# Kernel optimization log

Hardware: AMD Instinct MI355X
Metric: run time of the kernel (lower is better)

The kernel has to match this reference:

```python
import jax, jax.numpy as jnp
import numpy as np

D_IN = 1024
D_OUT = 1024
B = 4
S = 2048


def setup_inputs() -> dict:
    key = jax.random.key(0)
    kx, kq, kk, kv = jax.random.split(key, 4)
    x = jax.random.normal(kx, (B, S, D_IN), dtype=jnp.float32)
    # Linear weights stored as [d_in, d_out] so projection is x @ W
    sc = 1.0 / np.sqrt(D_IN)
    Wq = jax.random.normal(kq, (D_IN, D_OUT), dtype=jnp.float32) * sc
    Wk = jax.random.normal(kk, (D_IN, D_OUT), dtype=jnp.float32) * sc
    Wv = jax.random.normal(kv, (D_IN, D_OUT), dtype=jnp.float32) * sc
    return {"x": x, "Wq": Wq, "Wk": Wk, "Wv": Wv}


def reference(x, Wq, Wk, Wv):
    # q, k, v: [b, s, d_out]
    q = jnp.einsum("bsd,de->bse", x, Wq)
    k = jnp.einsum("bsd,de->bse", x, Wk)
    v = jnp.einsum("bsd,de->bse", x, Wv)
    s = q.shape[1]
    # raw scores [b, s, s]
    scores = jnp.einsum("bqd,bkd->bqk", q, k)
    # causal mask: disallow key j > query i (see notes re: original mask bug)
    causal = jnp.triu(jnp.ones((s, s), dtype=bool), k=1)
    scores = jnp.where(causal[None, :, :], -jnp.inf, scores)
    scale = 1.0 / jnp.sqrt(jnp.asarray(k.shape[-1], dtype=scores.dtype))
    att_weights = jax.nn.softmax(scores * scale, axis=-1)
    # dropout p=0.0 -> identity
    att_output = jnp.einsum("bqk,bkd->bqd", att_weights, v)
    return att_output, att_weights
```

## Files before the change

kernel.cpp:

```cpp
#include <hip/hip_runtime.h>
#include <stdint.h>

#define DIM 1024
#define SEQ 2048
#define NB 4

typedef unsigned short u16;
typedef __bf16 bf16x8 __attribute__((ext_vector_type(8)));
typedef float floatx4 __attribute__((ext_vector_type(4)));

__device__ __forceinline__ u16 f32_to_bf16(float f) {
  union { float f; unsigned u; } v; v.f = f;
  unsigned r = v.u + 0x7FFFu + ((v.u >> 16) & 1u);
  return (u16)(r >> 16);
}

__device__ __forceinline__ void async16(const void* g, void* l) {
  __builtin_amdgcn_global_load_lds(
      (__attribute__((address_space(1))) unsigned int*)g,
      (__attribute__((address_space(3))) unsigned int*)l, 16, 0, 0);
}

__global__ __launch_bounds__(256) void k_cvt(const float* __restrict__ src,
                                             u16* __restrict__ dst, int n4) {
  int i = blockIdx.x * blockDim.x + threadIdx.x;
  if (i >= n4) return;
  float4 v = ((const float4*)src)[i];
  ushort4 o;
  o.x = f32_to_bf16(v.x); o.y = f32_to_bf16(v.y);
  o.z = f32_to_bf16(v.z); o.w = f32_to_bf16(v.w);
  ((ushort4*)dst)[i] = o;
}

__global__ void k_tr_f32(const float* __restrict__ Wq, const float* __restrict__ Wk,
                         const float* __restrict__ Wv, u16* __restrict__ dst) {
  const int z = blockIdx.z;
  const float* src = (z == 0) ? Wq : (z == 1) ? Wk : Wv;
  u16* d = dst + (size_t)z * DIM * DIM;
  __shared__ u16 tile[32][33];
  int c0 = blockIdx.x * 32, r0 = blockIdx.y * 32;
  int tx = threadIdx.x, ty = threadIdx.y;
  #pragma unroll
  for (int dy = 0; dy < 32; dy += 8)
    tile[ty + dy][tx] = f32_to_bf16(src[(size_t)(r0 + ty + dy) * DIM + c0 + tx]);
  __syncthreads();
  #pragma unroll
  for (int dy = 0; dy < 32; dy += 8)
    d[(size_t)(c0 + ty + dy) * DIM + r0 + tx] = tile[tx][ty + dy];
}

__device__ __forceinline__ void mfma_core(const u16* __restrict__ A, int lda,
                                          const u16* __restrict__ Bt, int ldb,
                                          int ktiles, u16* lds,
                                          floatx4 acc[4][4]) {
  const int tid = threadIdx.x;
  const int lane = tid & 63;
  const int wid = tid >> 6;
  u16* lds_a = lds;
  u16* lds_b = lds + 8192;

  const u16* ag = A + (size_t)(wid * 32 + (lane >> 3)) * lda + (lane & 7) * 8;
  const u16* bg = Bt + (size_t)(wid * 32 + (lane >> 3)) * ldb + (lane & 7) * 8;
  u16* la = lds_a + wid * 2048;
  u16* lb = lds_b + wid * 2048;

  const int wm = (wid >> 1) * 64, wn = (wid & 1) * 64;
  const int lrow = lane & 15, quad = lane >> 4;
  const u16* pa = lds_a + (wm + lrow) * 64 + quad * 8;
  const u16* pb = lds_b + (wn + lrow) * 64 + quad * 8;

  for (int kt = 0; kt < ktiles; ++kt) {
    #pragma unroll
    for (int c = 0; c < 4; ++c) {
      async16(ag + (size_t)c * 8 * lda, la + c * 512);
      async16(bg + (size_t)c * 8 * ldb, lb + c * 512);
    }
    ag += 64; bg += 64;
    __syncthreads();
    #pragma unroll
    for (int ks = 0; ks < 2; ++ks) {
      bf16x8 af[4], bfr[4];
      #pragma unroll
      for (int t = 0; t < 4; ++t) af[t] = *(const bf16x8*)(pa + t * 1024 + ks * 32);
      #pragma unroll
      for (int t = 0; t < 4; ++t) bfr[t] = *(const bf16x8*)(pb + t * 1024 + ks * 32);
      #pragma unroll
      for (int i = 0; i < 4; ++i)
        #pragma unroll
        for (int j = 0; j < 4; ++j)
          acc[i][j] = __builtin_amdgcn_mfma_f32_16x16x32_bf16(af[i], bfr[j],
                                                              acc[i][j], 0, 0, 0);
    }
    __syncthreads();
  }
}

__global__ __launch_bounds__(256) void k_projqk(const u16* __restrict__ xb,
                                                const u16* __restrict__ wt,
                                                u16* __restrict__ qk) {
  const int x = blockIdx.x;
  const int mt = (x >> 7) * 8 + (x & 7);
  const int nt = (x >> 3) & 15;
  __shared__ u16 lds[16384];
  floatx4 acc[4][4] = {};
  mfma_core(xb + (size_t)mt * 128 * DIM, DIM,
            wt + (size_t)nt * 128 * DIM, DIM, DIM / 64, lds, acc);
  const int lane = threadIdx.x & 63, wid = threadIdx.x >> 6;
  const int wm = (wid >> 1) * 64, wn = (wid & 1) * 64;
  const int lrow = lane & 15, quad = lane >> 4;
  const int n0 = nt * 128;
  const int z = n0 >> 10;
  const int nn = n0 & 1023;
  u16* C = qk + (size_t)z * (NB * SEQ * DIM)
              + (size_t)(mt * 128 + wm + quad * 4) * DIM + nn + wn + lrow;
  #pragma unroll
  for (int i = 0; i < 4; ++i)
    #pragma unroll
    for (int r = 0; r < 4; ++r)
      #pragma unroll
      for (int j = 0; j < 4; ++j)
        C[(size_t)(i * 16 + r) * DIM + j * 16] = f32_to_bf16(acc[i][j][r]);
}

__global__ __launch_bounds__(256) void k_projv(const u16* __restrict__ wv,
                                               const u16* __restrict__ xb,
                                               u16* __restrict__ vT) {
  const int x = blockIdx.x;
  const int nt = (x >> 6) * 8 + (x & 7);
  const int mt = (x >> 3) & 7;
  __shared__ u16 lds[16384];
  floatx4 acc[4][4] = {};
  mfma_core(wv + (size_t)mt * 128 * DIM, DIM,
            xb + (size_t)nt * 128 * DIM, DIM, DIM / 64, lds, acc);
  const int lane = threadIdx.x & 63, wid = threadIdx.x >> 6;
  const int wm = (wid >> 1) * 64, wn = (wid & 1) * 64;
  const int lrow = lane & 15, quad = lane >> 4;
  const int t0 = nt * 128;
  const int b = t0 >> 11, s0 = t0 & 2047;
  u16* C = vT + (size_t)b * (DIM * SEQ)
              + (size_t)(mt * 128 + wm + quad * 4) * SEQ + s0 + wn + lrow;
  #pragma unroll
  for (int i = 0; i < 4; ++i)
    #pragma unroll
    for (int r = 0; r < 4; ++r)
      #pragma unroll
      for (int j = 0; j < 4; ++j)
        C[(size_t)(i * 16 + r) * SEQ + j * 16] = f32_to_bf16(acc[i][j][r]);
}

__global__ __launch_bounds__(256) void k_scores(const u16* __restrict__ q,
                                                const u16* __restrict__ k,
                                                float* __restrict__ w) {
  const int id = blockIdx.x;
  const int b = (id & 7) >> 1;
  const int mtl = id & 1;
  const int rest = id >> 3;
  const int mt = (rest >> 4) * 2 + mtl;
  const int nt = rest & 15;
  if (nt > mt) return;
  __shared__ u16 lds[16384];
  floatx4 acc[4][4] = {};
  mfma_core(q + (size_t)b * SEQ * DIM + (size_t)mt * 128 * DIM, DIM,
            k + (size_t)b * SEQ * DIM + (size_t)nt * 128 * DIM, DIM,
            DIM / 64, lds, acc);
  const int lane = threadIdx.x & 63, wid = threadIdx.x >> 6;
  const int wm = (wid >> 1) * 64, wn = (wid & 1) * 64;
  const int lrow = lane & 15, quad = lane >> 4;
  float* C = w + (size_t)b * SEQ * SEQ
               + (size_t)(mt * 128 + wm + quad * 4) * SEQ + nt * 128 + wn + lrow;
  #pragma unroll
  for (int i = 0; i < 4; ++i)
    #pragma unroll
    for (int r = 0; r < 4; ++r)
      #pragma unroll
      for (int j = 0; j < 4; ++j)
        C[(size_t)(i * 16 + r) * SEQ + j * 16] = acc[i][j][r] * 0.03125f;
}

__global__ __launch_bounds__(256) void k_softmax(float* __restrict__ w,
                                                 u16* __restrict__ P) {
  const int r = blockIdx.x;
  const int i = r & (SEQ - 1);
  const int len = i + 1;
  const int plen4 = (((i >> 7) + 1) << 7) >> 2;
  float4* srow = (float4*)(w + (size_t)r * SEQ);
  ushort4* prow = (ushort4*)(P + (size_t)r * SEQ);
  const int tid = threadIdx.x;
  const int lane = tid & 63, wid = tid >> 6;
  __shared__ float rm[4], rs[4];

  float4 e[2];
  float mx = -1e30f;
  #pragma unroll
  for (int u = 0; u < 2; ++u) {
    int q4 = tid + u * 256;
    int j0 = q4 * 4;
    float4 v = make_float4(-1e30f, -1e30f, -1e30f, -1e30f);
    if (j0 < len) {
      v = srow[q4];
      v.x = (j0 + 0 < len) ? v.x : -1e30f;
      v.y = (j0 + 1 < len) ? v.y : -1e30f;
      v.z = (j0 + 2 < len) ? v.z : -1e30f;
      v.w = (j0 + 3 < len) ? v.w : -1e30f;
    }
    e[u] = v;
    mx = fmaxf(mx, fmaxf(fmaxf(v.x, v.y), fmaxf(v.z, v.w)));
  }
  #pragma unroll
  for (int o = 32; o >= 1; o >>= 1) mx = fmaxf(mx, __shfl_xor(mx, o, 64));
  if (lane == 0) rm[wid] = mx;
  __syncthreads();
  mx = fmaxf(fmaxf(rm[0], rm[1]), fmaxf(rm[2], rm[3]));

  float sum = 0.f;
  #pragma unroll
  for (int u = 0; u < 2; ++u) {
    e[u].x = __expf(e[u].x - mx);
    e[u].y = __expf(e[u].y - mx);
    e[u].z = __expf(e[u].z - mx);
    e[u].w = __expf(e[u].w - mx);
    sum += e[u].x + e[u].y + e[u].z + e[u].w;
  }
  #pragma unroll
  for (int o = 32; o >= 1; o >>= 1) sum += __shfl_xor(sum, o, 64);
  if (lane == 0) rs[wid] = sum;
  __syncthreads();
  sum = rs[0] + rs[1] + rs[2] + rs[3];
  const float inv = 1.0f / sum;

  #pragma unroll
  for (int u = 0; u < 2; ++u) {
    int q4 = tid + u * 256;
    int j0 = q4 * 4;
    float4 v;
    v.x = (j0 + 0 < len) ? e[u].x * inv : 0.f;
    v.y = (j0 + 1 < len) ? e[u].y * inv : 0.f;
    v.z = (j0 + 2 < len) ? e[u].z * inv : 0.f;
    v.w = (j0 + 3 < len) ? e[u].w * inv : 0.f;
    srow[q4] = v;
    if (q4 < plen4) {
      ushort4 p;
      p.x = f32_to_bf16(v.x); p.y = f32_to_bf16(v.y);
      p.z = f32_to_bf16(v.z); p.w = f32_to_bf16(v.w);
      prow[q4] = p;
    }
  }
}

__global__ __launch_bounds__(256) void k_pv(const u16* __restrict__ P,
                                            const u16* __restrict__ vT,
                                            float* __restrict__ out) {
  const int id = blockIdx.x;
  const int b = (id & 7) >> 1;
  const int mtl = id & 1;
  const int rest = id >> 3;
  const int mt = (rest >> 3) * 2 + mtl;
  const int nt = rest & 7;
  __shared__ u16 lds[16384];
  floatx4 acc[4][4] = {};
  mfma_core(P + (size_t)b * SEQ * SEQ + (size_t)mt * 128 * SEQ, SEQ,
            vT + (size_t)b * DIM * SEQ + (size_t)nt * 128 * SEQ, SEQ,
            2 * (mt + 1), lds, acc);
  const int lane = threadIdx.x & 63, wid = threadIdx.x >> 6;
  const int wm = (wid >> 1) * 64, wn = (wid & 1) * 64;
  const int lrow = lane & 15, quad = lane >> 4;
  float* C = out + (size_t)b * SEQ * DIM
                 + (size_t)(mt * 128 + wm + quad * 4) * DIM + nt * 128 + wn + lrow;
  #pragma unroll
  for (int i = 0; i < 4; ++i)
    #pragma unroll
    for (int r = 0; r < 4; ++r)
      #pragma unroll
      for (int j = 0; j < 4; ++j)
        C[(size_t)(i * 16 + r) * DIM + j * 16] = acc[i][j][r];
}

extern "C" void kernel_launch(void* const* d_in, const int* in_sizes, int n_in,
                              void* d_out, int out_size, void* d_ws, size_t ws_size,
                              hipStream_t stream) {
  const float* x  = (const float*)d_in[0];
  const float* Wq = (const float*)d_in[1];
  const float* Wk = (const float*)d_in[2];
  const float* Wv = (const float*)d_in[3];
  float* att_out = (float*)d_out;
  float* att_w   = (float*)d_out + 8388608;

  u16* xb = (u16*)d_ws;
  u16* wt = xb + 8388608;
  u16* qk = wt + 3145728;
  u16* vT = qk + 16777216;
  u16* P  = vT + 8388608;

  dim3 tb(32, 8);
  k_cvt<<<8192, 256, 0, stream>>>(x, xb, 8388608 / 4);
  k_tr_f32<<<dim3(32, 32, 3), tb, 0, stream>>>(Wq, Wk, Wv, wt);
  k_projqk<<<1024, 256, 0, stream>>>(xb, wt, qk);
  k_projv<<<512, 256, 0, stream>>>(wt + 2097152, xb, vT);
  k_scores<<<1024, 256, 0, stream>>>(qk, qk + 8388608, att_w);
  k_softmax<<<8192, 256, 0, stream>>>(att_w, P);
  k_pv<<<512, 256, 0, stream>>>(P, vT, att_out);
}
```

Baseline: 316.7 us.

## Merge prep and projection launches, compact causal score grid, reorder PV blocks

Combines the x conversion and weight transpose into one launch, and the Q/K and V projections into one 1536-block launch, removing launch gaps and tail effects between them. The scores grid shrinks from 1024 blocks (half exiting early) to 544 blocks covering only lower-triangular tiles, using a sqrt-based triangular index. The PV kernel now schedules the longest row tiles first to improve load balance. Risks include losing the previous L2-friendly block swizzle and some integer/sqrt overhead per block.

```diff
diff --git a/kernel.cpp b/kernel.cpp
--- a/kernel.cpp
+++ b/kernel.cpp
@@ -21,32 +21,38 @@
       (__attribute__((address_space(3))) unsigned int*)l, 16, 0, 0);
 }
 
-__global__ __launch_bounds__(256) void k_cvt(const float* __restrict__ src,
-                                             u16* __restrict__ dst, int n4) {
-  int i = blockIdx.x * blockDim.x + threadIdx.x;
-  if (i >= n4) return;
-  float4 v = ((const float4*)src)[i];
-  ushort4 o;
-  o.x = f32_to_bf16(v.x); o.y = f32_to_bf16(v.y);
-  o.z = f32_to_bf16(v.z); o.w = f32_to_bf16(v.w);
-  ((ushort4*)dst)[i] = o;
-}
-
-__global__ void k_tr_f32(const float* __restrict__ Wq, const float* __restrict__ Wk,
-                         const float* __restrict__ Wv, u16* __restrict__ dst) {
-  const int z = blockIdx.z;
-  const float* src = (z == 0) ? Wq : (z == 1) ? Wk : Wv;
-  u16* d = dst + (size_t)z * DIM * DIM;
+__global__ __launch_bounds__(256) void k_prep(const float* __restrict__ x,
+                                              const float* __restrict__ Wq,
+                                              const float* __restrict__ Wk,
+                                              const float* __restrict__ Wv,
+                                              u16* __restrict__ xb,
+                                              u16* __restrict__ wt) {
   __shared__ u16 tile[32][33];
-  int c0 = blockIdx.x * 32, r0 = blockIdx.y * 32;
-  int tx = threadIdx.x, ty = threadIdx.y;
-  #pragma unroll
-  for (int dy = 0; dy < 32; dy += 8)
-    tile[ty + dy][tx] = f32_to_bf16(src[(size_t)(r0 + ty + dy) * DIM + c0 + tx]);
-  __syncthreads();
-  #pragma unroll
-  for (int dy = 0; dy < 32; dy += 8)
-    d[(size_t)(c0 + ty + dy) * DIM + r0 + tx] = tile[tx][ty + dy];
+  const int bid = blockIdx.x;
+  const int tid = threadIdx.x;
+  if (bid < 8192) {
+    int i = bid * 256 + tid;
+    float4 v = ((const float4*)x)[i];
+    ushort4 o;
+    o.x = f32_to_bf16(v.x); o.y = f32_to_bf16(v.y);
+    o.z = f32_to_bf16(v.z); o.w = f32_to_bf16(v.w);
+    ((ushort4*)xb)[i] = o;
+  } else {
+    int t = bid - 8192;
+    int z = t >> 10;
+    int ti = t & 1023;
+    int c0 = (ti & 31) * 32, r0 = (ti >> 5) * 32;
+    const float* src = (z == 0) ? Wq : (z == 1) ? Wk : Wv;
+    u16* d = wt + (size_t)z * DIM * DIM;
+    int tx = tid & 31, ty = tid >> 5;
+    #pragma unroll
+    for (int dy = 0; dy < 32; dy += 8)
+      tile[ty + dy][tx] = f32_to_bf16(src[(size_t)(r0 + ty + dy) * DIM + c0 + tx]);
+    __syncthreads();
+    #pragma unroll
+    for (int dy = 0; dy < 32; dy += 8)
+      d[(size_t)(c0 + ty + dy) * DIM + r0 + tx] = tile[tx][ty + dy];
+  }
 }
 
 __device__ __forceinline__ void mfma_core(const u16* __restrict__ A, int lda,
@@ -95,69 +101,64 @@
   }
 }
 
-__global__ __launch_bounds__(256) void k_projqk(const u16* __restrict__ xb,
-                                                const u16* __restrict__ wt,
-                                                u16* __restrict__ qk) {
-  const int x = blockIdx.x;
-  const int mt = (x >> 7) * 8 + (x & 7);
-  const int nt = (x >> 3) & 15;
+__global__ __launch_bounds__(256) void k_proj(const u16* __restrict__ xb,
+                                              const u16* __restrict__ wt,
+                                              u16* __restrict__ qk,
+                                              u16* __restrict__ vT) {
+  const int id = blockIdx.x;
+  const int z2 = id >> 9;
+  const int r = id & 511;
+  const int g = (r >> 6) * 8 + (r & 7);
+  const int h = (r >> 3) & 7;
   __shared__ u16 lds[16384];
   floatx4 acc[4][4] = {};
-  mfma_core(xb + (size_t)mt * 128 * DIM, DIM,
-            wt + (size_t)nt * 128 * DIM, DIM, DIM / 64, lds, acc);
+  const u16 *A, *Bt;
+  if (z2 < 2) {
+    A = xb + (size_t)g * 128 * DIM;
+    Bt = wt + (size_t)z2 * DIM * DIM + (size_t)h * 128 * DIM;
+  } else {
+    A = wt + (size_t)2 * DIM * DIM + (size_t)h * 128 * DIM;
+    Bt = xb + (size_t)g * 128 * DIM;
+  }
+  mfma_core(A, DIM, Bt, DIM, DIM / 64, lds, acc);
   const int lane = threadIdx.x & 63, wid = threadIdx.x >> 6;
   const int wm = (wid >> 1) * 64, wn = (wid & 1) * 64;
   const int lrow = lane & 15, quad = lane >> 4;
-  const int n0 = nt * 128;
-  const int z = n0 >> 10;
-  const int nn = n0 & 1023;
-  u16* C = qk + (size_t)z * (NB * SEQ * DIM)
-              + (size_t)(mt * 128 + wm + quad * 4) * DIM + nn + wn + lrow;
-  #pragma unroll
-  for (int i = 0; i < 4; ++i)
-    #pragma unroll
-    for (int r = 0; r < 4; ++r)
-      #pragma unroll
-      for (int j = 0; j < 4; ++j)
-        C[(size_t)(i * 16 + r) * DIM + j * 16] = f32_to_bf16(acc[i][j][r]);
-}
-
-__global__ __launch_bounds__(256) void k_projv(const u16* __restrict__ wv,
-                                               const u16* __restrict__ xb,
-                                               u16* __restrict__ vT) {
-  const int x = blockIdx.x;
-  const int nt = (x >> 6) * 8 + (x & 7);
-  const int mt = (x >> 3) & 7;
-  __shared__ u16 lds[16384];
-  floatx4 acc[4][4] = {};
-  mfma_core(wv + (size_t)mt * 128 * DIM, DIM,
-            xb + (size_t)nt * 128 * DIM, DIM, DIM / 64, lds, acc);
-  const int lane = threadIdx.x & 63, wid = threadIdx.x >> 6;
-  const int wm = (wid >> 1) * 64, wn = (wid & 1) * 64;
-  const int lrow = lane & 15, quad = lane >> 4;
-  const int t0 = nt * 128;
-  const int b = t0 >> 11, s0 = t0 & 2047;
-  u16* C = vT + (size_t)b * (DIM * SEQ)
-              + (size_t)(mt * 128 + wm + quad * 4) * SEQ + s0 + wn + lrow;
-  #pragma unroll
-  for (int i = 0; i < 4; ++i)
-    #pragma unroll
-    for (int r = 0; r < 4; ++r)
-      #pragma unroll
-      for (int j = 0; j < 4; ++j)
-        C[(size_t)(i * 16 + r) * SEQ + j * 16] = f32_to_bf16(acc[i][j][r]);
+  if (z2 < 2) {
+    u16* C = qk + (size_t)z2 * (NB * SEQ * DIM)
+                + (size_t)(g * 128 + wm + quad * 4) * DIM + h * 128 + wn + lrow;
+    #pragma unroll
+    for (int i = 0; i < 4; ++i)
+      #pragma unroll
+      for (int rr = 0; rr < 4; ++rr)
+        #pragma unroll
+        for (int j = 0; j < 4; ++j)
+          C[(size_t)(i * 16 + rr) * DIM + j * 16] = f32_to_bf16(acc[i][j][rr]);
+  } else {
+    const int t0 = g * 128;
+    const int b = t0 >> 11, s0 = t0 & 2047;
+    u16* C = vT + (size_t)b * (DIM * SEQ)
+                + (size_t)(h * 128 + wm + quad * 4) * SEQ + s0 + wn + lrow;
+    #pragma unroll
+    for (int i = 0; i < 4; ++i)
+      #pragma unroll
+      for (int rr = 0; rr < 4; ++rr)
+        #pragma unroll
+        for (int j = 0; j < 4; ++j)
+          C[(size_t)(i * 16 + rr) * SEQ + j * 16] = f32_to_bf16(acc[i][j][rr]);
+  }
 }
 
 __global__ __launch_bounds__(256) void k_scores(const u16* __restrict__ q,
                                                 const u16* __restrict__ k,
                                                 float* __restrict__ w) {
   const int id = blockIdx.x;
-  const int b = (id & 7) >> 1;
-  const int mtl = id & 1;
-  const int rest = id >> 3;
-  const int mt = (rest >> 4) * 2 + mtl;
-  const int nt = rest & 15;
-  if (nt > mt) return;
+  const int b = id & 3;
+  int t = id >> 2;
+  int mt = (int)((sqrtf(8.0f * (float)t + 1.0f) - 1.0f) * 0.5f);
+  while ((mt + 1) * (mt + 2) / 2 <= t) ++mt;
+  while (mt * (mt + 1) / 2 > t) --mt;
+  const int nt = t - mt * (mt + 1) / 2;
   __shared__ u16 lds[16384];
   floatx4 acc[4][4] = {};
   mfma_core(q + (size_t)b * SEQ * DIM + (size_t)mt * 128 * DIM, DIM,
@@ -171,10 +172,10 @@
   #pragma unroll
   for (int i = 0; i < 4; ++i)
     #pragma unroll
-    for (int r = 0; r < 4; ++r)
+    for (int rr = 0; rr < 4; ++rr)
       #pragma unroll
       for (int j = 0; j < 4; ++j)
-        C[(size_t)(i * 16 + r) * SEQ + j * 16] = acc[i][j][r] * 0.03125f;
+        C[(size_t)(i * 16 + rr) * SEQ + j * 16] = acc[i][j][rr] * 0.03125f;
 }
 
 __global__ __launch_bounds__(256) void k_softmax(float* __restrict__ w,
@@ -251,11 +252,9 @@
                                             const u16* __restrict__ vT,
                                             float* __restrict__ out) {
   const int id = blockIdx.x;
-  const int b = (id & 7) >> 1;
-  const int mtl = id & 1;
-  const int rest = id >> 3;
-  const int mt = (rest >> 3) * 2 + mtl;
-  const int nt = rest & 7;
+  const int mt = 15 - (id >> 5);
+  const int nt = (id >> 2) & 7;
+  const int b = id & 3;
   __shared__ u16 lds[16384];
   floatx4 acc[4][4] = {};
   mfma_core(P + (size_t)b * SEQ * SEQ + (size_t)mt * 128 * SEQ, SEQ,
@@ -269,10 +268,10 @@
   #pragma unroll
   for (int i = 0; i < 4; ++i)
     #pragma unroll
-    for (int r = 0; r < 4; ++r)
+    for (int rr = 0; rr < 4; ++rr)
       #pragma unroll
       for (int j = 0; j < 4; ++j)
-        C[(size_t)(i * 16 + r) * DIM + j * 16] = acc[i][j][r];
+        C[(size_t)(i * 16 + rr) * DIM + j * 16] = acc[i][j][rr];
 }
 
 extern "C" void kernel_launch(void* const* d_in, const int* in_sizes, int n_in,
@@ -291,12 +290,9 @@
   u16* vT = qk + 16777216;
   u16* P  = vT + 8388608;
 
-  dim3 tb(32, 8);
-  k_cvt<<<8192, 256, 0, stream>>>(x, xb, 8388608 / 4);
-  k_tr_f32<<<dim3(32, 32, 3), tb, 0, stream>>>(Wq, Wk, Wv, wt);
-  k_projqk<<<1024, 256, 0, stream>>>(xb, wt, qk);
-  k_projv<<<512, 256, 0, stream>>>(wt + 2097152, xb, vT);
-  k_scores<<<1024, 256, 0, stream>>>(qk, qk + 8388608, att_w);
+  k_prep<<<11264, 256, 0, stream>>>(x, Wq, Wk, Wv, xb, wt);
+  k_proj<<<1536, 256, 0, stream>>>(xb, wt, qk, vT);
+  k_scores<<<544, 256, 0, stream>>>(qk, qk + 8388608, att_w);
   k_softmax<<<8192, 256, 0, stream>>>(att_w, P);
   k_pv<<<512, 256, 0, stream>>>(P, vT, att_out);
 }
```

New measurement: 304.9 us. 3.7% less time.
